# Optimization experiments

Hardware: AMD Instinct MI355X
Metric: run time of the kernel (lower is better)

## Reference

```python
import jax, jax.numpy as jnp
import numpy as np
import math

H = 64   # hidden_size
N = 512  # num_objects
B = 128  # batch


def setup_inputs() -> dict:
    key = jax.random.key(0)
    ks = jax.random.split(key, 10)
    q = jax.random.normal(ks[0], (N, B, H), dtype=jnp.float32)
    k = jax.random.normal(ks[1], (N, B, H), dtype=jnp.float32)
    v = jax.random.normal(ks[2], (N, B, H), dtype=jnp.float32)
    # binary visibility mask [B, N, N]
    batch_traffic_id_map = (jax.random.uniform(ks[3], (B, N, N)) < 0.7).astype(jnp.float32)
    s = 1.0 / math.sqrt(H)
    Wq = jax.random.uniform(ks[4], (H, H), minval=-s, maxval=s, dtype=jnp.float32)
    bq = jax.random.uniform(ks[5], (H,), minval=-s, maxval=s, dtype=jnp.float32)
    Wk = jax.random.uniform(ks[6], (H, H), minval=-s, maxval=s, dtype=jnp.float32)
    bk = jax.random.uniform(ks[7], (H,), minval=-s, maxval=s, dtype=jnp.float32)
    Wv = jax.random.uniform(ks[8], (H, H), minval=-s, maxval=s, dtype=jnp.float32)
    bv = jax.random.uniform(ks[9], (H,), minval=-s, maxval=s, dtype=jnp.float32)
    return {"q": q, "k": k, "v": v, "batch_traffic_id_map": batch_traffic_id_map,
            "Wq": Wq, "bq": bq, "Wk": Wk, "bk": bk, "Wv": Wv, "bv": bv}


def reference(q, k, v, batch_traffic_id_map, Wq, bq, Wk, bk, Wv, bv):
    hidden_size = q.shape[-1]
    # Linear projections then transpose(0,1): [N,B,H] -> [B,N,H]
    qp = jnp.einsum('nbh,kh->bnk', q, Wq) + bq
    kp = jnp.einsum('nbh,kh->bnk', k, Wk) + bk
    vp = jnp.einsum('nbh,kh->bnk', v, Wv) + bv
    # scaled scores, exp, mask, custom sum-normalization
    a = jnp.einsum('bnh,bmh->bnm', qp, kp) / jnp.sqrt(jnp.float32(hidden_size))
    a = jnp.exp(a) * batch_traffic_id_map
    a_sum = jnp.sum(a, axis=-1)                      # [B, N]
    a_sum = jnp.where(a_sum == 0, jnp.ones_like(a_sum), a_sum)
    A = a / a_sum[..., None]                          # [B, N, N]
    out = jnp.einsum('bnm,bmh->nbh', A, vp)           # matmul + transpose(0,1)
    # dropout is identity in eval mode
    return out, A
```

## Files before the change

kernel.cpp:

```cpp
#include <hip/hip_runtime.h>

#define H 64
#define NOBJ 512
#define BATCH 128
#define PACK_BLOCKS ((BATCH * NOBJ * NOBJ) / 1024)

typedef __attribute__((ext_vector_type(8))) short s16x8;
typedef __attribute__((ext_vector_type(4))) float f32x4;
typedef __attribute__((ext_vector_type(4))) unsigned short u16x4;
typedef __attribute__((ext_vector_type(8))) unsigned short u16x8;

__device__ __forceinline__ unsigned short f2bf(float f) {
    unsigned int u = __float_as_uint(f);
    u += 0x7FFFu + ((u >> 16) & 1u);
    return (unsigned short)(u >> 16);
}
__device__ __forceinline__ float bf2f(unsigned short h) {
    return __uint_as_float((unsigned int)h << 16);
}

#define MFMA16(a, b, c) __builtin_amdgcn_mfma_f32_16x16x32_bf16(a, b, c, 0, 0, 0)
#define SBAR() __builtin_amdgcn_sched_barrier(0)

__global__ __launch_bounds__(256) void prep_kernel(
    const float* __restrict__ mask, unsigned int* __restrict__ bits,
    const float* __restrict__ q, const float* __restrict__ k, const float* __restrict__ v,
    const float* __restrict__ Wq, const float* __restrict__ bq,
    const float* __restrict__ Wk, const float* __restrict__ bk,
    const float* __restrict__ Wv, const float* __restrict__ bv,
    unsigned short* __restrict__ qh, unsigned short* __restrict__ ql,
    unsigned short* __restrict__ kh, unsigned short* __restrict__ kl,
    unsigned short* __restrict__ vt)
{
    __shared__ unsigned short vtile[64][72];
    const int tid = threadIdx.x;

    if (blockIdx.x < PACK_BLOCKS) {
        unsigned char* nib = (unsigned char*)&vtile[0][0];
        const size_t base = (size_t)blockIdx.x * 1024;
        const f32x4 f = __builtin_nontemporal_load((const f32x4*)(mask + base + (size_t)tid * 4));
        nib[tid] = (unsigned char)((unsigned)(f[0] != 0.0f)
                 | ((unsigned)(f[1] != 0.0f) << 1)
                 | ((unsigned)(f[2] != 0.0f) << 2)
                 | ((unsigned)(f[3] != 0.0f) << 3));
        __syncthreads();
        if (tid < 32) {
            unsigned int wv = 0;
            #pragma unroll
            for (int i = 0; i < 8; ++i)
                wv |= (unsigned int)nib[tid * 8 + i] << (4 * i);
            bits[base / 32 + tid] = wv;
        }
        return;
    }

    const int p   = blockIdx.x - PACK_BLOCKS;
    const int z   = p >> 10;
    const int rem = p & 1023;
    const int b   = rem >> 3;
    const int n0  = (rem & 7) * 64;

    const float* x; const float* W; const float* bias;
    unsigned short* yh; unsigned short* yl;
    if (z == 0)      { x = q; W = Wq; bias = bq; yh = qh; yl = ql; }
    else if (z == 1) { x = k; W = Wk; bias = bk; yh = kh; yl = kl; }
    else             { x = v; W = Wv; bias = bv; yh = nullptr; yl = nullptr; }

    const int lane = tid & 63;
    const int wt   = tid >> 6;
    const int l15  = lane & 15;
    const int lg   = lane >> 4;

    s16x8 wfh[4][2], wfl[4][2];
    #pragma unroll
    for (int ht = 0; ht < 4; ++ht) {
        #pragma unroll
        for (int kc = 0; kc < 2; ++kc) {
            const float* wp = W + (ht * 16 + l15) * H + kc * 32 + lg * 8;
            float4 f0 = *(const float4*)wp;
            float4 f1 = *(const float4*)(wp + 4);
            float f[8] = {f0.x, f0.y, f0.z, f0.w, f1.x, f1.y, f1.z, f1.w};
            s16x8 hi8, lo8;
            #pragma unroll
            for (int j = 0; j < 8; ++j) {
                const unsigned short hb = f2bf(f[j]);
                hi8[j] = (short)hb;
                lo8[j] = (short)f2bf(f[j] - bf2f(hb));
            }
            wfh[ht][kc] = hi8; wfl[ht][kc] = lo8;
        }
    }

    const int n = n0 + wt * 16 + l15;
    const float* xr = x + ((size_t)n * BATCH + b) * H;
    s16x8 xfh[2], xfl[2];
    #pragma unroll
    for (int kc = 0; kc < 2; ++kc) {
        const float* xp = xr + kc * 32 + lg * 8;
        float4 f0 = *(const float4*)xp;
        float4 f1 = *(const float4*)(xp + 4);
        float f[8] = {f0.x, f0.y, f0.z, f0.w, f1.x, f1.y, f1.z, f1.w};
        s16x8 hi8, lo8;
        #pragma unroll
        for (int j = 0; j < 8; ++j) {
            const unsigned short hb = f2bf(f[j]);
            hi8[j] = (short)hb;
            lo8[j] = (short)f2bf(f[j] - bf2f(hb));
        }
        xfh[kc] = hi8; xfl[kc] = lo8;
    }

    if (z < 2) {
        #pragma unroll
        for (int ht = 0; ht < 4; ++ht) {
            const float4 b4 = *(const float4*)(bias + ht * 16 + lg * 4);
            f32x4 acc = {b4.x, b4.y, b4.z, b4.w};
            acc = MFMA16(wfh[ht][0], xfh[0], acc);
            acc = MFMA16(wfh[ht][1], xfh[1], acc);
            acc = MFMA16(wfh[ht][0], xfl[0], acc);
            acc = MFMA16(wfh[ht][1], xfl[1], acc);
            acc = MFMA16(wfl[ht][0], xfh[0], acc);
            acc = MFMA16(wfl[ht][1], xfh[1], acc);
            u16x4 hv, lv;
            #pragma unroll
            for (int r = 0; r < 4; ++r) {
                const unsigned short hb = f2bf(acc[r]);
                hv[r] = hb;
                lv[r] = f2bf(acc[r] - bf2f(hb));
            }
            const size_t o = ((size_t)b * NOBJ + n) * H + ht * 16 + lg * 4;
            *(u16x4*)(yh + o) = hv;
            *(u16x4*)(yl + o) = lv;
        }
    } else {
        #pragma unroll
        for (int ht = 0; ht < 4; ++ht) {
            const float bs = bias[ht * 16 + l15];
            f32x4 acc = {bs, bs, bs, bs};
            acc = MFMA16(xfh[0], wfh[ht][0], acc);
            acc = MFMA16(xfh[1], wfh[ht][1], acc);
            acc = MFMA16(xfl[0], wfh[ht][0], acc);
            acc = MFMA16(xfl[1], wfh[ht][1], acc);
            acc = MFMA16(xfh[0], wfl[ht][0], acc);
            acc = MFMA16(xfh[1], wfl[ht][1], acc);
            u16x4 hv;
            #pragma unroll
            for (int r = 0; r < 4; ++r) hv[r] = f2bf(acc[r]);
            *(u16x4*)&vtile[ht * 16 + l15][wt * 16 + lg * 4] = hv;
        }
        __syncthreads();
        const int h = tid >> 2, nc = (tid & 3) * 16;
        const u16x8 d0 = *(const u16x8*)&vtile[h][nc];
        const u16x8 d1 = *(const u16x8*)&vtile[h][nc + 8];
        unsigned short* dst = vt + ((size_t)b * H + h) * NOBJ + n0 + nc;
        *(u16x8*)dst = d0;
        *(u16x8*)(dst + 8) = d1;
    }
}

__global__ __launch_bounds__(256, 2) void attn_kernel(
    const unsigned short* __restrict__ qh, const unsigned short* __restrict__ ql,
    const unsigned short* __restrict__ kh, const unsigned short* __restrict__ kl,
    const unsigned short* __restrict__ vt, const unsigned int* __restrict__ bits,
    float* __restrict__ out, float* __restrict__ Aout)
{
    __shared__ unsigned short sch[16][520];
    __shared__ unsigned short scl[16][520];
    __shared__ float rsum[4][16];
    __shared__ float inv[16];

    const int tid  = threadIdx.x;
    const int lane = tid & 63;
    const int w    = tid >> 6;
    const int l15  = lane & 15;
    const int lg   = lane >> 4;

    const int orig = blockIdx.x;
    const int xcd  = orig & 7;
    const int s    = orig >> 3;
    const int b    = xcd + 8 * (s >> 5);
    const int n0   = (s & 31) * 16;

    const size_t qoff = ((size_t)b * NOBJ + n0 + l15) * H + lg * 8;
    const s16x8 qfh0 = *(const s16x8*)(qh + qoff);
    const s16x8 qfh1 = *(const s16x8*)(qh + qoff + 32);
    const s16x8 qfl0 = *(const s16x8*)(ql + qoff);
    const s16x8 qfl1 = *(const s16x8*)(ql + qoff + 32);

    const unsigned short* khp = kh + ((size_t)b * NOBJ + w * 128 + l15) * H + lg * 8;
    const unsigned short* klp = kl + ((size_t)b * NOBJ + w * 128 + l15) * H + lg * 8;

    const uint4 mw = *(const uint4*)(bits + ((size_t)b * NOBJ + n0 + l15) * (NOBJ / 32) + w * 4);
    const unsigned mwa[4] = {mw.x, mw.y, mw.z, mw.w};

    float rp = 0.0f;

    s16x8 kA[2][4], kB[2][4];

#define LOADP(dst, mt0)                                                   \
    do {                                                                  \
        dst[0][0] = *(const s16x8*)(khp + (mt0) * 16 * H);                \
        dst[0][1] = *(const s16x8*)(khp + (mt0) * 16 * H + 32);           \
        dst[0][2] = *(const s16x8*)(klp + (mt0) * 16 * H);                \
        dst[0][3] = *(const s16x8*)(klp + (mt0) * 16 * H + 32);           \
        dst[1][0] = *(const s16x8*)(khp + ((mt0) + 1) * 16 * H);          \
        dst[1][1] = *(const s16x8*)(khp + ((mt0) + 1) * 16 * H + 32);     \
        dst[1][2] = *(const s16x8*)(klp + ((mt0) + 1) * 16 * H);          \
        dst[1][3] = *(const s16x8*)(klp + ((mt0) + 1) * 16 * H + 32);     \
    } while (0)

#define SCORE1(src, i, mt)                                                \
    do {                                                                  \
        f32x4 acc = {0.0f, 0.0f, 0.0f, 0.0f};                             \
        acc = MFMA16(src[i][0], qfh0, acc);                               \
        acc = MFMA16(src[i][1], qfh1, acc);                               \
        acc = MFMA16(src[i][0], qfl0, acc);                               \
        acc = MFMA16(src[i][1], qfl1, acc);                               \
        acc = MFMA16(src[i][2], qfh0, acc);                               \
        acc = MFMA16(src[i][3], qfh1, acc);                               \
        const unsigned wsel = mwa[(mt) >> 1] >> ((((mt) & 1) << 4) + (lg << 2)); \
        u16x4 hv, lv;                                                     \
        _Pragma("unroll")                                                 \
        for (int r = 0; r < 4; ++r) {                                     \
            const float ex = __expf(acc[r] * 0.125f);                     \
            const float e = ((wsel >> r) & 1u) ? ex : 0.0f;               \
            rp += e;                                                      \
            const unsigned short hb = f2bf(e);                            \
            hv[r] = hb;                                                   \
            lv[r] = f2bf(e - bf2f(hb));                                   \
        }                                                                 \
        const int mo = w * 128 + (mt) * 16 + lg * 4;                      \
        *(u16x4*)&sch[l15][mo] = hv;                                      \
        *(u16x4*)&scl[l15][mo] = lv;                                      \
    } while (0)

    LOADP(kA, 0);
    SBAR();
    LOADP(kB, 2);
    SBAR();
    SCORE1(kA, 0, 0); SCORE1(kA, 1, 1);
    LOADP(kA, 4);
    SBAR();
    SCORE1(kB, 0, 2); SCORE1(kB, 1, 3);
    LOADP(kB, 6);
    SBAR();
    SCORE1(kA, 0, 4); SCORE1(kA, 1, 5);
    SCORE1(kB, 0, 6); SCORE1(kB, 1, 7);
#undef LOADP
#undef SCORE1

    const unsigned short* vtp = vt + ((size_t)b * H + w * 16 + l15) * NOBJ + lg * 8;
    s16x8 vA0, vA1, vB0, vB1;
    vA0 = *(const s16x8*)(vtp);
    vA1 = *(const s16x8*)(vtp + 32);
    SBAR();

    rp += __shfl_xor(rp, 16);
    rp += __shfl_xor(rp, 32);
    if (lane < 16) rsum[w][lane] = rp;
    __syncthreads();
    if (tid < 16) {
        const float sv = (rsum[0][tid] + rsum[1][tid]) + (rsum[2][tid] + rsum[3][tid]);
        inv[tid] = 1.0f / (sv == 0.0f ? 1.0f : sv);
    }
    __syncthreads();

    {
        const float iv = inv[l15];
        float* Arow = Aout + ((size_t)b * NOBJ + n0 + l15) * NOBJ + w * 128 + lg * 4;
        #pragma unroll
        for (int mt = 0; mt < 8; ++mt) {
            const int mo = w * 128 + mt * 16 + lg * 4;
            const u16x4 hv = *(const u16x4*)&sch[l15][mo];
            const u16x4 lv = *(const u16x4*)&scl[l15][mo];
            float4 a4;
            a4.x = (bf2f(hv[0]) + bf2f(lv[0])) * iv;
            a4.y = (bf2f(hv[1]) + bf2f(lv[1])) * iv;
            a4.z = (bf2f(hv[2]) + bf2f(lv[2])) * iv;
            a4.w = (bf2f(hv[3]) + bf2f(lv[3])) * iv;
            *(float4*)(Arow + mt * 16) = a4;
        }
    }

    f32x4 o0 = {0.0f, 0.0f, 0.0f, 0.0f}, o1 = {0.0f, 0.0f, 0.0f, 0.0f};

#define LOADV(d0, d1, ks)                                                 \
    do {                                                                  \
        d0 = *(const s16x8*)(vtp + (ks) * 32);                            \
        d1 = *(const s16x8*)(vtp + (ks) * 32 + 32);                       \
    } while (0)

#define AVSTEP(v0, v1, ks)                                                \
    do {                                                                  \
        const int mk = (ks) * 32 + lg * 8;                                \
        const s16x8 ah0 = *(const s16x8*)&sch[l15][mk];                   \
        const s16x8 al0 = *(const s16x8*)&scl[l15][mk];                   \
        o0 = MFMA16(ah0, v0, o0);                                         \
        o0 = MFMA16(al0, v0, o0);                                         \
        const s16x8 ah1 = *(const s16x8*)&sch[l15][mk + 32];              \
        const s16x8 al1 = *(const s16x8*)&scl[l15][mk + 32];              \
        o1 = MFMA16(ah1, v1, o1);                                         \
        o1 = MFMA16(al1, v1, o1);                                         \
    } while (0)

    LOADV(vB0, vB1, 2);  SBAR();
    AVSTEP(vA0, vA1, 0);
    LOADV(vA0, vA1, 4);  SBAR();
    AVSTEP(vB0, vB1, 2);
    LOADV(vB0, vB1, 6);  SBAR();
    AVSTEP(vA0, vA1, 4);
    LOADV(vA0, vA1, 8);  SBAR();
    AVSTEP(vB0, vB1, 6);
    LOADV(vB0, vB1, 10); SBAR();
    AVSTEP(vA0, vA1, 8);
    LOADV(vA0, vA1, 12); SBAR();
    AVSTEP(vB0, vB1, 10);
    LOADV(vB0, vB1, 14); SBAR();
    AVSTEP(vA0, vA1, 12);
    AVSTEP(vB0, vB1, 14);
#undef LOADV
#undef AVSTEP

    #pragma unroll
    for (int r = 0; r < 4; ++r) {
        const int nn = lg * 4 + r;
        out[((size_t)(n0 + nn) * BATCH + b) * H + w * 16 + l15] = (o0[r] + o1[r]) * inv[nn];
    }
}

extern "C" void kernel_launch(void* const* d_in, const int* in_sizes, int n_in,
                              void* d_out, int out_size, void* d_ws, size_t ws_size,
                              hipStream_t stream)
{
    (void)in_sizes; (void)n_in; (void)out_size; (void)ws_size;
    const float* q    = (const float*)d_in[0];
    const float* k    = (const float*)d_in[1];
    const float* v    = (const float*)d_in[2];
    const float* mask = (const float*)d_in[3];
    const float* Wq   = (const float*)d_in[4];
    const float* bq   = (const float*)d_in[5];
    const float* Wk   = (const float*)d_in[6];
    const float* bk   = (const float*)d_in[7];
    const float* Wv   = (const float*)d_in[8];
    const float* bv   = (const float*)d_in[9];

    float* out  = (float*)d_out;
    float* Aout = (float*)d_out + (size_t)NOBJ * BATCH * H;

    const size_t S = (size_t)BATCH * NOBJ * H;
    unsigned short* qh = (unsigned short*)d_ws;
    unsigned short* ql = qh + S;
    unsigned short* kh = ql + S;
    unsigned short* kl = kh + S;
    unsigned short* vt = kl + S;
    unsigned int* bits = (unsigned int*)(vt + S);

    prep_kernel<<<dim3(PACK_BLOCKS + 3 * BATCH * (NOBJ / 64)), 256, 0, stream>>>(
        mask, bits, q, k, v, Wq, bq, Wk, bk, Wv, bv, qh, ql, kh, kl, vt);
    attn_kernel<<<dim3((NOBJ / 16) * BATCH), 256, 0, stream>>>(
        qh, ql, kh, kl, vt, bits, out, Aout);
}
```

Measured before the change: 401.2 us.

## Store Q/K/V projections in MFMA fragment order and widen A-row stores

```diff
diff --git a/kernel.cpp b/kernel.cpp
--- a/kernel.cpp
+++ b/kernel.cpp
@@ -21,6 +21,7 @@
 
 #define MFMA16(a, b, c) __builtin_amdgcn_mfma_f32_16x16x32_bf16(a, b, c, 0, 0, 0)
 #define SBAR() __builtin_amdgcn_sched_barrier(0)
+
 
 __global__ __launch_bounds__(256) void prep_kernel(
     const float* __restrict__ mask, unsigned int* __restrict__ bits,
@@ -28,9 +29,9 @@
     const float* __restrict__ Wq, const float* __restrict__ bq,
     const float* __restrict__ Wk, const float* __restrict__ bk,
     const float* __restrict__ Wv, const float* __restrict__ bv,
-    unsigned short* __restrict__ qh, unsigned short* __restrict__ ql,
-    unsigned short* __restrict__ kh, unsigned short* __restrict__ kl,
-    unsigned short* __restrict__ vt)
+    unsigned short* __restrict__ qhf, unsigned short* __restrict__ qlf,
+    unsigned short* __restrict__ khf, unsigned short* __restrict__ klf,
+    unsigned short* __restrict__ vtf)
 {
     __shared__ unsigned short vtile[64][72];
     const int tid = threadIdx.x;
@@ -62,21 +63,21 @@
 
     const float* x; const float* W; const float* bias;
     unsigned short* yh; unsigned short* yl;
-    if (z == 0)      { x = q; W = Wq; bias = bq; yh = qh; yl = ql; }
-    else if (z == 1) { x = k; W = Wk; bias = bk; yh = kh; yl = kl; }
+    if (z == 0)      { x = q; W = Wq; bias = bq; yh = qhf; yl = qlf; }
+    else if (z == 1) { x = k; W = Wk; bias = bk; yh = khf; yl = klf; }
     else             { x = v; W = Wv; bias = bv; yh = nullptr; yl = nullptr; }
 
     const int lane = tid & 63;
     const int wt   = tid >> 6;
-    const int l15  = lane & 15;
-    const int lg   = lane >> 4;
+    const int pl   = lane & 15;
+    const int pg   = lane >> 4;
 
     s16x8 wfh[4][2], wfl[4][2];
     #pragma unroll
     for (int ht = 0; ht < 4; ++ht) {
         #pragma unroll
         for (int kc = 0; kc < 2; ++kc) {
-            const float* wp = W + (ht * 16 + l15) * H + kc * 32 + lg * 8;
+            const float* wp = W + (ht * 16 + pl) * H + kc * 32 + pg * 8;
             float4 f0 = *(const float4*)wp;
             float4 f1 = *(const float4*)(wp + 4);
             float f[8] = {f0.x, f0.y, f0.z, f0.w, f1.x, f1.y, f1.z, f1.w};
@@ -91,12 +92,12 @@
         }
     }
 
-    const int n = n0 + wt * 16 + l15;
+    const int n = n0 + wt * 16 + pl;
     const float* xr = x + ((size_t)n * BATCH + b) * H;
     s16x8 xfh[2], xfl[2];
     #pragma unroll
     for (int kc = 0; kc < 2; ++kc) {
-        const float* xp = xr + kc * 32 + lg * 8;
+        const float* xp = xr + kc * 32 + pg * 8;
         float4 f0 = *(const float4*)xp;
         float4 f1 = *(const float4*)(xp + 4);
         float f[8] = {f0.x, f0.y, f0.z, f0.w, f1.x, f1.y, f1.z, f1.w};
@@ -113,7 +114,7 @@
     if (z < 2) {
         #pragma unroll
         for (int ht = 0; ht < 4; ++ht) {
-            const float4 b4 = *(const float4*)(bias + ht * 16 + lg * 4);
+            const float4 b4 = *(const float4*)(bias + ht * 16 + pg * 4);
             f32x4 acc = {b4.x, b4.y, b4.z, b4.w};
             acc = MFMA16(wfh[ht][0], xfh[0], acc);
             acc = MFMA16(wfh[ht][1], xfh[1], acc);
@@ -128,14 +129,19 @@
                 hv[r] = hb;
                 lv[r] = f2bf(acc[r] - bf2f(hb));
             }
-            const size_t o = ((size_t)b * NOBJ + n) * H + ht * 16 + lg * 4;
-            *(u16x4*)(yh + o) = hv;
-            *(u16x4*)(yl + o) = lv;
+            const int g   = ht * 4 + pg;
+            const int kc  = g >> 3;
+            const int lgA = (g >> 1) & 3;
+            const int jh  = g & 1;
+            const size_t off = ((size_t)(b * 32 + (n0 >> 4) + wt) * 2 + kc) * 512
+                             + (lgA * 16 + pl) * 8 + jh * 4;
+            *(u16x4*)(yh + off) = hv;
+            *(u16x4*)(yl + off) = lv;
         }
     } else {
         #pragma unroll
         for (int ht = 0; ht < 4; ++ht) {
-            const float bs = bias[ht * 16 + l15];
+            const float bs = bias[ht * 16 + pl];
             f32x4 acc = {bs, bs, bs, bs};
             acc = MFMA16(xfh[0], wfh[ht][0], acc);
             acc = MFMA16(xfh[1], wfh[ht][1], acc);
@@ -146,22 +152,27 @@
             u16x4 hv;
             #pragma unroll
             for (int r = 0; r < 4; ++r) hv[r] = f2bf(acc[r]);
-            *(u16x4*)&vtile[ht * 16 + l15][wt * 16 + lg * 4] = hv;
+            *(u16x4*)&vtile[ht * 16 + pl][wt * 16 + pg * 4] = hv;
         }
         __syncthreads();
-        const int h = tid >> 2, nc = (tid & 3) * 16;
-        const u16x8 d0 = *(const u16x8*)&vtile[h][nc];
-        const u16x8 d1 = *(const u16x8*)&vtile[h][nc + 8];
-        unsigned short* dst = vt + ((size_t)b * H + h) * NOBJ + n0 + nc;
-        *(u16x8*)dst = d0;
-        *(u16x8*)(dst + 8) = d1;
+        #pragma unroll
+        for (int i = 0; i < 2; ++i) {
+            const int c     = tid * 2 + i;
+            const int laneA = c & 63;
+            const int ksl   = (c >> 6) & 1;
+            const int hw    = c >> 7;
+            const u16x8 d = *(const u16x8*)&vtile[hw * 16 + (laneA & 15)]
+                                                 [ksl * 32 + ((laneA >> 4) & 3) * 8];
+            *(u16x8*)(vtf + (((size_t)(b * 4 + hw) * 16) + (n0 >> 5) + ksl) * 512
+                          + laneA * 8) = d;
+        }
     }
 }
 
 __global__ __launch_bounds__(256, 2) void attn_kernel(
-    const unsigned short* __restrict__ qh, const unsigned short* __restrict__ ql,
-    const unsigned short* __restrict__ kh, const unsigned short* __restrict__ kl,
-    const unsigned short* __restrict__ vt, const unsigned int* __restrict__ bits,
+    const unsigned short* __restrict__ qhf, const unsigned short* __restrict__ qlf,
+    const unsigned short* __restrict__ khf, const unsigned short* __restrict__ klf,
+    const unsigned short* __restrict__ vtf, const unsigned int* __restrict__ bits,
     float* __restrict__ out, float* __restrict__ Aout)
 {
     __shared__ unsigned short sch[16][520];
@@ -179,16 +190,18 @@
     const int xcd  = orig & 7;
     const int s    = orig >> 3;
     const int b    = xcd + 8 * (s >> 5);
-    const int n0   = (s & 31) * 16;
-
-    const size_t qoff = ((size_t)b * NOBJ + n0 + l15) * H + lg * 8;
-    const s16x8 qfh0 = *(const s16x8*)(qh + qoff);
-    const s16x8 qfh1 = *(const s16x8*)(qh + qoff + 32);
-    const s16x8 qfl0 = *(const s16x8*)(ql + qoff);
-    const s16x8 qfl1 = *(const s16x8*)(ql + qoff + 32);
-
-    const unsigned short* khp = kh + ((size_t)b * NOBJ + w * 128 + l15) * H + lg * 8;
-    const unsigned short* klp = kl + ((size_t)b * NOBJ + w * 128 + l15) * H + lg * 8;
+    const int nt   = s & 31;
+    const int n0   = nt * 16;
+
+    const unsigned short* qbase_h = qhf + ((size_t)(b * 32 + nt)) * 1024 + lane * 8;
+    const unsigned short* qbase_l = qlf + ((size_t)(b * 32 + nt)) * 1024 + lane * 8;
+    const s16x8 qfh0 = *(const s16x8*)(qbase_h);
+    const s16x8 qfh1 = *(const s16x8*)(qbase_h + 512);
+    const s16x8 qfl0 = *(const s16x8*)(qbase_l);
+    const s16x8 qfl1 = *(const s16x8*)(qbase_l + 512);
+
+    const unsigned short* khfp = khf + ((size_t)(b * 32 + w * 8)) * 1024 + lane * 8;
+    const unsigned short* klfp = klf + ((size_t)(b * 32 + w * 8)) * 1024 + lane * 8;
 
     const uint4 mw = *(const uint4*)(bits + ((size_t)b * NOBJ + n0 + l15) * (NOBJ / 32) + w * 4);
     const unsigned mwa[4] = {mw.x, mw.y, mw.z, mw.w};
@@ -199,14 +212,14 @@
 
 #define LOADP(dst, mt0)                                                   \
     do {                                                                  \
-        dst[0][0] = *(const s16x8*)(khp + (mt0) * 16 * H);                \
-        dst[0][1] = *(const s16x8*)(khp + (mt0) * 16 * H + 32);           \
-        dst[0][2] = *(const s16x8*)(klp + (mt0) * 16 * H);                \
-        dst[0][3] = *(const s16x8*)(klp + (mt0) * 16 * H + 32);           \
-        dst[1][0] = *(const s16x8*)(khp + ((mt0) + 1) * 16 * H);          \
-        dst[1][1] = *(const s16x8*)(khp + ((mt0) + 1) * 16 * H + 32);     \
-        dst[1][2] = *(const s16x8*)(klp + ((mt0) + 1) * 16 * H);          \
-        dst[1][3] = *(const s16x8*)(klp + ((mt0) + 1) * 16 * H + 32);     \
+        dst[0][0] = *(const s16x8*)(khfp + (mt0) * 1024);                 \
+        dst[0][1] = *(const s16x8*)(khfp + (mt0) * 1024 + 512);           \
+        dst[0][2] = *(const s16x8*)(klfp + (mt0) * 1024);                 \
+        dst[0][3] = *(const s16x8*)(klfp + (mt0) * 1024 + 512);           \
+        dst[1][0] = *(const s16x8*)(khfp + ((mt0) + 1) * 1024);           \
+        dst[1][1] = *(const s16x8*)(khfp + ((mt0) + 1) * 1024 + 512);     \
+        dst[1][2] = *(const s16x8*)(klfp + ((mt0) + 1) * 1024);           \
+        dst[1][3] = *(const s16x8*)(klfp + ((mt0) + 1) * 1024 + 512);     \
     } while (0)
 
 #define SCORE1(src, i, mt)                                                \
@@ -249,10 +262,10 @@
 #undef LOADP
 #undef SCORE1
 
-    const unsigned short* vtp = vt + ((size_t)b * H + w * 16 + l15) * NOBJ + lg * 8;
+    const unsigned short* vtfp = vtf + ((size_t)(b * 4 + w) * 16) * 512 + lane * 8;
     s16x8 vA0, vA1, vB0, vB1;
-    vA0 = *(const s16x8*)(vtp);
-    vA1 = *(const s16x8*)(vtp + 32);
+    vA0 = *(const s16x8*)(vtfp);
+    vA1 = *(const s16x8*)(vtfp + 512);
     SBAR();
 
     rp += __shfl_xor(rp, 16);
@@ -266,19 +279,24 @@
     __syncthreads();
 
     {
-        const float iv = inv[l15];
-        float* Arow = Aout + ((size_t)b * NOBJ + n0 + l15) * NOBJ + w * 128 + lg * 4;
-        #pragma unroll
-        for (int mt = 0; mt < 8; ++mt) {
-            const int mo = w * 128 + mt * 16 + lg * 4;
-            const u16x4 hv = *(const u16x4*)&sch[l15][mo];
-            const u16x4 lv = *(const u16x4*)&scl[l15][mo];
-            float4 a4;
-            a4.x = (bf2f(hv[0]) + bf2f(lv[0])) * iv;
-            a4.y = (bf2f(hv[1]) + bf2f(lv[1])) * iv;
-            a4.z = (bf2f(hv[2]) + bf2f(lv[2])) * iv;
-            a4.w = (bf2f(hv[3]) + bf2f(lv[3])) * iv;
-            *(float4*)(Arow + mt * 16) = a4;
+        const int row = tid >> 4, t16 = tid & 15;
+        const float iv = inv[row];
+        float* Arow = Aout + ((size_t)b * NOBJ + n0 + row) * NOBJ + t16 * 32;
+        #pragma unroll
+        for (int cc = 0; cc < 4; ++cc) {
+            const u16x8 hv = *(const u16x8*)&sch[row][t16 * 32 + cc * 8];
+            const u16x8 lv = *(const u16x8*)&scl[row][t16 * 32 + cc * 8];
+            float4 a0, a1;
+            a0.x = (bf2f(hv[0]) + bf2f(lv[0])) * iv;
+            a0.y = (bf2f(hv[1]) + bf2f(lv[1])) * iv;
+            a0.z = (bf2f(hv[2]) + bf2f(lv[2])) * iv;
+            a0.w = (bf2f(hv[3]) + bf2f(lv[3])) * iv;
+            a1.x = (bf2f(hv[4]) + bf2f(lv[4])) * iv;
+            a1.y = (bf2f(hv[5]) + bf2f(lv[5])) * iv;
+            a1.z = (bf2f(hv[6]) + bf2f(lv[6])) * iv;
+            a1.w = (bf2f(hv[7]) + bf2f(lv[7])) * iv;
+            *(float4*)(Arow + cc * 8)     = a0;
+            *(float4*)(Arow + cc * 8 + 4) = a1;
         }
     }
 
@@ -286,8 +304,8 @@
 
 #define LOADV(d0, d1, ks)                                                 \
     do {                                                                  \
-        d0 = *(const s16x8*)(vtp + (ks) * 32);                            \
-        d1 = *(const s16x8*)(vtp + (ks) * 32 + 32);                       \
+        d0 = *(const s16x8*)(vtfp + (ks) * 512);                          \
+        d1 = *(const s16x8*)(vtfp + ((ks) + 1) * 512);                    \
     } while (0)
 
 #define AVSTEP(v0, v1, ks)                                                \
@@ -348,15 +366,15 @@
     float* Aout = (float*)d_out + (size_t)NOBJ * BATCH * H;
 
     const size_t S = (size_t)BATCH * NOBJ * H;
-    unsigned short* qh = (unsigned short*)d_ws;
-    unsigned short* ql = qh + S;
-    unsigned short* kh = ql + S;
-    unsigned short* kl = kh + S;
-    unsigned short* vt = kl + S;
-    unsigned int* bits = (unsigned int*)(vt + S);
+    unsigned short* qhf = (unsigned short*)d_ws;
+    unsigned short* qlf = qhf + S;
+    unsigned short* khf = qlf + S;
+    unsigned short* klf = khf + S;
+    unsigned short* vtf = klf + S;
+    unsigned int* bits = (unsigned int*)(vtf + S);
 
     prep_kernel<<<dim3(PACK_BLOCKS + 3 * BATCH * (NOBJ / 64)), 256, 0, stream>>>(
-        mask, bits, q, k, v, Wq, bq, Wk, bk, Wv, bv, qh, ql, kh, kl, vt);
+        mask, bits, q, k, v, Wq, bq, Wk, bk, Wv, bv, qhf, qlf, khf, klf, vtf);
     attn_kernel<<<dim3((NOBJ / 16) * BATCH), 256, 0, stream>>>(
-        qh, ql, kh, kl, vt, bits, out, Aout);
-}
+        qhf, qlf, khf, klf, vtf, bits, out, Aout);
+}
```

After: 362.0 us. 1.11x faster.
